# Kernel tuning notes

Hardware: AMD Instinct MI355X
Metric: run time of the kernel (lower is better)

The kernel has to match this reference:

```python
import jax, jax.numpy as jnp
import numpy as np

D_MODEL = 256
NHEAD = 8
HEAD_DIM = D_MODEL // NHEAD
EPS_ATTN = 1e-6
EPS_LN = 1e-5


def _layernorm(x, g, b):
    mu = jnp.mean(x, axis=-1, keepdims=True)
    var = jnp.mean(jnp.square(x - mu), axis=-1, keepdims=True)
    return (x - mu) * jax.lax.rsqrt(var + EPS_LN) * g + b


def _embed_rotary(t, cos, sin):
    # t, cos, sin: [N, L, C]; interleaved pair rotation as in RoFPE.embed_rotary
    t2 = jnp.stack([-t[..., 1::2], t[..., ::2]], axis=-1).reshape(t.shape)
    return t * cos + t2 * sin


def setup_inputs() -> dict:
    key = jax.random.key(0)
    ks = jax.random.split(key, 12)
    N, L, S, C = 4, 4800, 4800, D_MODEL
    w = lambda k, shp: jax.random.normal(k, shp, dtype=jnp.float32) * 0.05
    return {
        "x": jax.random.normal(ks[0], (N, L, C), dtype=jnp.float32),
        "source": jax.random.normal(ks[1], (N, S, C), dtype=jnp.float32),
        "x_pe": jax.random.normal(ks[2], (N, L, C, 2), dtype=jnp.float32),
        "source_pe": jax.random.normal(ks[3], (N, S, C, 2), dtype=jnp.float32),
        "Wq": w(ks[4], (C, C)),
        "Wk": w(ks[5], (C, C)),
        "Wv": w(ks[6], (C, C)),
        "Wm": w(ks[7], (C, C)),
        "W1": w(ks[8], (2 * C, 2 * C)),
        "W2": w(ks[9], (C, 2 * C)),
        "g1": jnp.ones((C,), dtype=jnp.float32),
        "b1": jnp.zeros((C,), dtype=jnp.float32),
        "g2": jnp.ones((C,), dtype=jnp.float32),
        "b2": jnp.zeros((C,), dtype=jnp.float32),
    }


def reference(x, source, x_pe, source_pe, Wq, Wk, Wv, Wm, W1, W2, g1, b1, g2, b2):
    bs, L, C = x.shape
    H, D = NHEAD, HEAD_DIM
    # projections (nn.Linear: y = x @ W.T)
    q = x @ Wq.T
    k = source @ Wk.T
    v = source @ Wv.T
    # inline rotary PE
    q = _embed_rotary(q, x_pe[..., 0], x_pe[..., 1]).reshape(bs, L, H, D)
    k = _embed_rotary(k, source_pe[..., 0], source_pe[..., 1]).reshape(bs, -1, H, D)
    v = v.reshape(bs, -1, H, D)
    # LoFTR linear attention: phi(x) = elu(x) + 1
    Q = jax.nn.elu(q) + 1.0
    K = jax.nn.elu(k) + 1.0
    v_len = v.shape[1]
    vals = v / v_len
    KV = jnp.einsum("nshd,nshv->nhdv", K, vals)          # [N,H,D,D]
    Z = 1.0 / (jnp.einsum("nlhd,nhd->nlh", Q, K.sum(axis=1)) + EPS_ATTN)
    msg = jnp.einsum("nlhd,nhdv,nlh->nlhv", Q, KV, Z) * v_len  # [N,L,H,D]
    # merge + norm1
    msg = msg.reshape(bs, L, H * D) @ Wm.T
    msg = _layernorm(msg, g1, b1)
    # concat-MLP + norm2 + residual
    h = jnp.concatenate([x, msg], axis=-1)               # [N,L,2C]
    h = jax.nn.relu(h @ W1.T) @ W2.T
    h = _layernorm(h, g2, b2)
    return x + h
```

## Files before the change

### kernel.cpp

```cpp
#include <hip/hip_runtime.h>
#include <hip/hip_bf16.h>
#include <math.h>

#define NROWS 19200
#define SLEN  4800
#define KV_CHUNKS 50
#define KV_SC     96

typedef unsigned short ushort_t;
typedef __attribute__((ext_vector_type(8))) short bf16x8;
typedef __attribute__((ext_vector_type(4))) float f32x4;
typedef __attribute__((ext_vector_type(8))) unsigned short ushort8;

__device__ __forceinline__ float bf2f(ushort_t u) {
  union { unsigned int i; float f; } x; x.i = ((unsigned int)u) << 16; return x.f;
}
__device__ __forceinline__ ushort_t f2bf(float f) {
  __hip_bfloat16 h = __float2bfloat16(f);
  union { __hip_bfloat16 h; ushort_t u; } x; x.h = h; return x.u;
}

#define GLOAD16(g, l) __builtin_amdgcn_global_load_lds( \
    (const __attribute__((address_space(1))) unsigned int*)(g), \
    (__attribute__((address_space(3))) unsigned int*)(l), 16, 0, 0)

template <int EPI, bool CONCAT>
__device__ __forceinline__ void gemmT_body(
    const ushort_t* __restrict__ A0, const ushort_t* __restrict__ A1,
    const ushort_t* __restrict__ W, ushort_t* __restrict__ outp,
    int Nn, int K, int bm, int bn, char* smem) {
  const int tid = threadIdx.x;
  const int wave = tid >> 6, lane = tid & 63;
  const int wm = (wave >> 1) * 64, wn = (wave & 1) * 64;
  const int l15 = lane & 15, l4 = lane >> 4;

  f32x4 acc[4][4];
#pragma unroll
  for (int i = 0; i < 4; ++i)
#pragma unroll
    for (int j = 0; j < 4; ++j) acc[i][j] = (f32x4){0.f, 0.f, 0.f, 0.f};

  for (int k0 = 0; k0 < K; k0 += 64) {
    const ushort_t* Asrc;
    int ka;
    if (CONCAT) { Asrc = (k0 < 256) ? A0 : A1; ka = k0 & 255; }
    else        { Asrc = A0; ka = k0; }
#pragma unroll
    for (int c = 0; c < 4; ++c) {
      int ch = c * 4 + wave;
      int o = ch * 1024 + lane * 16;
      int row = o >> 7, g = (o >> 4) & 7;
      const ushort_t* sp =
          Asrc + (size_t)(bm + row) * 256 + ka + ((g ^ (row & 7)) << 3);
      GLOAD16(sp, smem + ch * 1024);
    }
#pragma unroll
    for (int c = 0; c < 4; ++c) {
      int ch = c * 4 + wave;
      int o = ch * 1024 + lane * 16;
      int row = o >> 7, g = (o >> 4) & 7;
      const ushort_t* sp =
          W + (size_t)(bn + row) * K + k0 + ((g ^ (row & 7)) << 3);
      GLOAD16(sp, smem + 16384 + ch * 1024);
    }
    __syncthreads();
#pragma unroll
    for (int kc = 0; kc < 2; ++kc) {
      bf16x8 af[4], bfr[4];
#pragma unroll
      for (int mi = 0; mi < 4; ++mi) {
        int r = wm + mi * 16 + l15;
        int G = kc * 4 + l4;
        af[mi] = *(const bf16x8*)(smem + r * 128 + ((G ^ (r & 7)) << 4));
      }
#pragma unroll
      for (int ni = 0; ni < 4; ++ni) {
        int r = wn + ni * 16 + l15;
        int G = kc * 4 + l4;
        bfr[ni] = *(const bf16x8*)(smem + 16384 + r * 128 +
                                   ((G ^ (r & 7)) << 4));
      }
#pragma unroll
      for (int mi = 0; mi < 4; ++mi)
#pragma unroll
        for (int ni = 0; ni < 4; ++ni)
          acc[mi][ni] = __builtin_amdgcn_mfma_f32_16x16x32_bf16(
              af[mi], bfr[ni], acc[mi][ni], 0, 0, 0);
    }
    __syncthreads();
  }

  ushort_t* st = (ushort_t*)smem;
#pragma unroll
  for (int mi = 0; mi < 4; ++mi)
#pragma unroll
    for (int ni = 0; ni < 4; ++ni)
#pragma unroll
      for (int j = 0; j < 4; ++j) {
        int trow = wm + mi * 16 + l4 * 4 + j;
        int tcol = wn + ni * 16 + l15;
        float v = acc[mi][ni][j];
        if (EPI == 3) v = fmaxf(v, 0.f);
        st[trow * 140 + tcol] = f2bf(v);
      }
  __syncthreads();
#pragma unroll
  for (int c = 0; c < 8; ++c) {
    int ch = c * 256 + tid;
    int row = ch >> 4, g = ch & 15;
    ushort8 u = *(const ushort8*)&st[row * 140 + g * 8];
    *(ushort8*)&outp[(size_t)(bm + row) * Nn + bn + g * 8] = u;
  }
}

__global__ __launch_bounds__(256) void qkv_fused(
    const ushort_t* __restrict__ xb, const ushort_t* __restrict__ srcb,
    const ushort_t* __restrict__ Wqb, const ushort_t* __restrict__ Wkb,
    const ushort_t* __restrict__ Wvb,
    ushort_t* __restrict__ Q, ushort_t* __restrict__ Kb,
    ushort_t* __restrict__ Vb) {
  extern __shared__ char smem[];
  int b = blockIdx.x;
  const int which = b < 300 ? 0 : (b < 600 ? 1 : 2);
  b -= which * 300;
  const int bm = (b >> 1) * 128, bn = (b & 1) * 128;
  const ushort_t* A = (which == 0) ? xb : srcb;
  const ushort_t* W = (which == 0) ? Wqb : (which == 1 ? Wkb : Wvb);
  ushort_t* o = (which == 0) ? Q : (which == 1 ? Kb : Vb);
  gemmT_body<0, false>(A, nullptr, W, o, 256, 256, bm, bn, smem);
}

__global__ __launch_bounds__(256) void mlp1_kernel(
    const ushort_t* __restrict__ xb, const ushort_t* __restrict__ msgln,
    const ushort_t* __restrict__ W1b, ushort_t* __restrict__ h1) {
  extern __shared__ char smem[];
  const int bm = (blockIdx.x >> 2) * 128, bn = (blockIdx.x & 3) * 128;
  gemmT_body<3, true>(xb, msgln, W1b, h1, 512, 512, bm, bn, smem);
}

__global__ __launch_bounds__(256) void msg_merge_ln(
    const ushort_t* __restrict__ Qb, const float* __restrict__ x_pe,
    const float* __restrict__ KV, const float* __restrict__ Ksum,
    const ushort_t* __restrict__ Wm,
    const float* __restrict__ g, const float* __restrict__ bb,
    ushort_t* __restrict__ msgln) {
  __shared__ ushort_t AsM[32 * 256];
  __shared__ ushort_t KVb[8 * 1024];
  __shared__ ushort_t Bs[256 * 32];
  __shared__ float Ks[8][32];
  __shared__ float zS[32][8];
  __shared__ float partS[4][32];
  __shared__ float partQ[4][32];
  __shared__ float gS[256], bS[256];

  const int tid = threadIdx.x;
  const int wave = tid >> 6, lane = tid & 63;
  const int l15 = lane & 15, l4 = lane >> 4;
  const int bm = blockIdx.x * 32;
  const int n = bm / SLEN;

  gS[tid] = g[tid];
  bS[tid] = bb[tid];
  Ks[tid >> 5][tid & 31] = Ksum[(n * 8 + (tid >> 5)) * 32 + (tid & 31)];

#pragma unroll
  for (int c = 0; c < 8; ++c) {
    int e4 = c * 256 + tid;
    const float4 kv4 = *(const float4*)&KV[(size_t)(n * 8) * 1024 + e4 * 4];
    ushort4 u = make_ushort4(f2bf(kv4.x), f2bf(kv4.y), f2bf(kv4.z),
                             f2bf(kv4.w));
    *(ushort4*)&KVb[e4 * 4] = u;
  }

#pragma unroll
  for (int p = 0; p < 4; ++p) {
    int rr = p * 8 + (tid >> 5), cc = (tid & 31) * 8;
    const size_t eoff = (size_t)(bm + rr) * 256 + cc;
    const ushort8 uq = *(const ushort8*)&Qb[eoff];
    const float4* pp = (const float4*)&x_pe[eoff * 2];
    float4 p0 = pp[0], p1 = pp[1], p2 = pp[2], p3 = pp[3];
    float v[8];
#pragma unroll
    for (int i = 0; i < 8; ++i) v[i] = bf2f((ushort_t)uq[i]);
    float r[8];
    r[0] = v[0] * p0.x - v[1] * p0.y; r[1] = v[1] * p0.z + v[0] * p0.w;
    r[2] = v[2] * p1.x - v[3] * p1.y; r[3] = v[3] * p1.z + v[2] * p1.w;
    r[4] = v[4] * p2.x - v[5] * p2.y; r[5] = v[5] * p2.z + v[4] * p2.w;
    r[6] = v[6] * p3.x - v[7] * p3.y; r[7] = v[7] * p3.z + v[6] * p3.w;
    ushort8 pk;
#pragma unroll
    for (int i = 0; i < 8; ++i) {
      float w = r[i] > 0.f ? r[i] + 1.f : __expf(r[i]);
      pk[i] = f2bf(w);
    }
    int gi = cc >> 3;
    int gis = (gi & ~7) | ((gi & 7) ^ (rr & 7));
    *(ushort8*)&AsM[rr * 256 + gis * 8] = pk;
  }
  __syncthreads();

  {
    int row = tid >> 3, h = tid & 7;
    float z = 0.f;
#pragma unroll
    for (int d = 0; d < 32; ++d) {
      int gi = h * 4 + (d >> 3);
      int gis = (gi & ~7) | ((gi & 7) ^ (row & 7));
      z += bf2f(AsM[row * 256 + gis * 8 + (d & 7)]) * Ks[h][d];
    }
    zS[row][h] = 1.0f / (z + 1e-6f);
  }
  __syncthreads();

  f32x4 macc[2][2][2];
#pragma unroll
  for (int hh2 = 0; hh2 < 2; ++hh2) {
    const int h = wave * 2 + hh2;
    bf16x8 af[2], bfr[2];
#pragma unroll
    for (int mi = 0; mi < 2; ++mi) {
      int r = mi * 16 + l15;
      int gi = h * 4 + l4;
      int gis = (gi & ~7) | ((gi & 7) ^ (r & 7));
      af[mi] = *(const bf16x8*)&AsM[r * 256 + gis * 8];
    }
#pragma unroll
    for (int ni = 0; ni < 2; ++ni) {
      int v = ni * 16 + l15;
      const ushort_t* kvb = &KVb[h * 1024 + v];
      bf16x8 t;
#pragma unroll
      for (int i = 0; i < 8; ++i) t[i] = (short)kvb[(l4 * 8 + i) * 32];
      bfr[ni] = t;
    }
#pragma unroll
    for (int mi = 0; mi < 2; ++mi)
#pragma unroll
      for (int ni = 0; ni < 2; ++ni)
        macc[hh2][mi][ni] = __builtin_amdgcn_mfma_f32_16x16x32_bf16(
            af[mi], bfr[ni], (f32x4){0.f, 0.f, 0.f, 0.f}, 0, 0, 0);
  }
  __syncthreads();

#pragma unroll
  for (int hh2 = 0; hh2 < 2; ++hh2) {
    const int h = wave * 2 + hh2;
#pragma unroll
    for (int mi = 0; mi < 2; ++mi)
#pragma unroll
      for (int ni = 0; ni < 2; ++ni)
#pragma unroll
        for (int j = 0; j < 4; ++j) {
          int row = mi * 16 + l4 * 4 + j;
          int col = h * 32 + ni * 16 + l15;
          float mv = macc[hh2][mi][ni][j] * zS[row][h];
          int gi = col >> 3;
          int gis = (gi & ~7) | ((gi & 7) ^ (row & 7));
          AsM[row * 256 + gis * 8 + (col & 7)] = f2bf(mv);
        }
  }
  __syncthreads();

  f32x4 acc[2][4];
#pragma unroll
  for (int i = 0; i < 2; ++i)
#pragma unroll
    for (int j = 0; j < 4; ++j) acc[i][j] = (f32x4){0.f, 0.f, 0.f, 0.f};

  for (int k0 = 0; k0 < 256; k0 += 32) {
#pragma unroll
    for (int c = 0; c < 4; ++c) {
      int ch = c * 256 + tid;
      int row = ch >> 2, gch = ch & 3;
      const ushort_t* src =
          Wm + (size_t)row * 256 + k0 + ((gch ^ (row & 3)) << 3);
      GLOAD16(src, (char*)Bs + ch * 16);
    }
    __syncthreads();
    bf16x8 af[2], bfr[4];
#pragma unroll
    for (int mi = 0; mi < 2; ++mi) {
      int r = mi * 16 + l15;
      int gi = (k0 >> 3) + l4;
      int gis = (gi & ~7) | ((gi & 7) ^ (r & 7));
      af[mi] = *(const bf16x8*)&AsM[r * 256 + gis * 8];
    }
#pragma unroll
    for (int ni = 0; ni < 4; ++ni) {
      int r = wave * 64 + ni * 16 + l15;
      int gs = l4 ^ (r & 3);
      bfr[ni] = *(const bf16x8*)&Bs[r * 32 + gs * 8];
    }
#pragma unroll
    for (int mi = 0; mi < 2; ++mi)
#pragma unroll
      for (int ni = 0; ni < 4; ++ni)
        acc[mi][ni] = __builtin_amdgcn_mfma_f32_16x16x32_bf16(
            af[mi], bfr[ni], acc[mi][ni], 0, 0, 0);
    __syncthreads();
  }

#pragma unroll
  for (int mi = 0; mi < 2; ++mi)
#pragma unroll
    for (int j = 0; j < 4; ++j) {
      float s = acc[mi][0][j] + acc[mi][1][j] + acc[mi][2][j] + acc[mi][3][j];
      float q = acc[mi][0][j] * acc[mi][0][j] + acc[mi][1][j] * acc[mi][1][j] +
                acc[mi][2][j] * acc[mi][2][j] + acc[mi][3][j] * acc[mi][3][j];
#pragma unroll
      for (int m = 1; m < 16; m <<= 1) {
        s += __shfl_xor(s, m);
        q += __shfl_xor(q, m);
      }
      if (l15 == 0) {
        int row = mi * 16 + l4 * 4 + j;
        partS[wave][row] = s;
        partQ[wave][row] = q;
      }
    }
  __syncthreads();

  float mu[2][4], rsv[2][4];
#pragma unroll
  for (int mi = 0; mi < 2; ++mi)
#pragma unroll
    for (int j = 0; j < 4; ++j) {
      int row = mi * 16 + l4 * 4 + j;
      float s = partS[0][row] + partS[1][row] + partS[2][row] + partS[3][row];
      float q2 = partQ[0][row] + partQ[1][row] + partQ[2][row] + partQ[3][row];
      float m_ = s * (1.f / 256.f);
      float var = q2 * (1.f / 256.f) - m_ * m_;
      mu[mi][j] = m_;
      rsv[mi][j] = rsqrtf(var + 1e-5f);
    }

#pragma unroll
  for (int mi = 0; mi < 2; ++mi)
#pragma unroll
    for (int ni = 0; ni < 4; ++ni)
#pragma unroll
      for (int j = 0; j < 4; ++j) {
        int row = mi * 16 + l4 * 4 + j;
        int col2 = wave * 64 + ni * 16 + l15;
        float vv = (acc[mi][ni][j] - mu[mi][j]) * rsv[mi][j] * gS[col2] +
                   bS[col2];
        msgln[(size_t)(bm + row) * 256 + col2] = f2bf(vv);
      }
}

template <int KDIM, bool RESID, bool OUTBF>
__global__ __launch_bounds__(256) void gemm_ln_kernel(
    const ushort_t* __restrict__ A, const ushort_t* __restrict__ W,
    const float* __restrict__ g, const float* __restrict__ bb,
    const float* __restrict__ resid, void* __restrict__ outp) {
  __shared__ char As[32 * 128];
  __shared__ char Bs[256 * 128];
  __shared__ float partS[4][32];
  __shared__ float partQ[4][32];
  __shared__ float gS[256], bS[256];

  const int tid = threadIdx.x;
  const int wave = tid >> 6, lane = tid & 63;
  const int l15 = lane & 15, l4 = lane >> 4;
  const int bm = blockIdx.x * 32;

  gS[tid] = g[tid];
  bS[tid] = bb[tid];

  f32x4 acc[2][4];
#pragma unroll
  for (int i = 0; i < 2; ++i)
#pragma unroll
    for (int j = 0; j < 4; ++j) acc[i][j] = (f32x4){0.f, 0.f, 0.f, 0.f};

  for (int k0 = 0; k0 < KDIM; k0 += 64) {
    {
      int row = tid >> 3, gch = tid & 7;
      const ushort_t* src =
          A + (size_t)(bm + row) * KDIM + k0 + ((gch ^ (row & 7)) << 3);
      GLOAD16(src, As + tid * 16);
    }
#pragma unroll
    for (int c = 0; c < 8; ++c) {
      int ch = c * 256 + tid;
      int row = ch >> 3, gch = ch & 7;
      const ushort_t* src =
          W + (size_t)row * KDIM + k0 + ((gch ^ (row & 7)) << 3);
      GLOAD16(src, Bs + ch * 16);
    }
    __syncthreads();
#pragma unroll
    for (int kc = 0; kc < 2; ++kc) {
      bf16x8 af[2], bfr[4];
#pragma unroll
      for (int mi = 0; mi < 2; ++mi) {
        int r = mi * 16 + l15;
        int G = kc * 4 + l4;
        af[mi] = *(const bf16x8*)(As + r * 128 + ((G ^ (r & 7)) << 4));
      }
#pragma unroll
      for (int ni = 0; ni < 4; ++ni) {
        int r = wave * 64 + ni * 16 + l15;
        int G = kc * 4 + l4;
        bfr[ni] = *(const bf16x8*)(Bs + r * 128 + ((G ^ (r & 7)) << 4));
      }
#pragma unroll
      for (int mi = 0; mi < 2; ++mi)
#pragma unroll
        for (int ni = 0; ni < 4; ++ni)
          acc[mi][ni] = __builtin_amdgcn_mfma_f32_16x16x32_bf16(
              af[mi], bfr[ni], acc[mi][ni], 0, 0, 0);
    }
    __syncthreads();
  }

#pragma unroll
  for (int mi = 0; mi < 2; ++mi)
#pragma unroll
    for (int j = 0; j < 4; ++j) {
      float s = acc[mi][0][j] + acc[mi][1][j] + acc[mi][2][j] + acc[mi][3][j];
      float q = acc[mi][0][j] * acc[mi][0][j] + acc[mi][1][j] * acc[mi][1][j] +
                acc[mi][2][j] * acc[mi][2][j] + acc[mi][3][j] * acc[mi][3][j];
#pragma unroll
      for (int m = 1; m < 16; m <<= 1) {
        s += __shfl_xor(s, m);
        q += __shfl_xor(q, m);
      }
      if (l15 == 0) {
        int row = mi * 16 + l4 * 4 + j;
        partS[wave][row] = s;
        partQ[wave][row] = q;
      }
    }
  __syncthreads();

  float mu[2][4], rsv[2][4];
#pragma unroll
  for (int mi = 0; mi < 2; ++mi)
#pragma unroll
    for (int j = 0; j < 4; ++j) {
      int row = mi * 16 + l4 * 4 + j;
      float s = partS[0][row] + partS[1][row] + partS[2][row] + partS[3][row];
      float q2 = partQ[0][row] + partQ[1][row] + partQ[2][row] + partQ[3][row];
      float m_ = s * (1.f / 256.f);
      float var = q2 * (1.f / 256.f) - m_ * m_;
      mu[mi][j] = m_;
      rsv[mi][j] = rsqrtf(var + 1e-5f);
    }

#pragma unroll
  for (int mi = 0; mi < 2; ++mi)
#pragma unroll
    for (int ni = 0; ni < 4; ++ni)
#pragma unroll
      for (int j = 0; j < 4; ++j) {
        int row = mi * 16 + l4 * 4 + j;
        int col = wave * 64 + ni * 16 + l15;
        float v = (acc[mi][ni][j] - mu[mi][j]) * rsv[mi][j] * gS[col] + bS[col];
        size_t gr = (size_t)(bm + row);
        if (RESID) v += resid[gr * 256 + col];
        if (OUTBF)
          ((ushort_t*)outp)[gr * 256 + col] = f2bf(v);
        else
          ((float*)outp)[gr * 256 + col] = v;
      }
}

__global__ __launch_bounds__(256) void kv_partial(
    const ushort_t* __restrict__ Kb, const ushort_t* __restrict__ Vb,
    const float* __restrict__ s_pe,
    float* __restrict__ kvp, float* __restrict__ ksp) {
  __shared__ float bufK[32][32];
  __shared__ float bufV[32][32];
  const int b = blockIdx.x;
  const int ch = b % KV_CHUNKS;
  const int nh = b / KV_CHUNKS;
  const int h = nh & 7, n = nh >> 3;
  const int tid = threadIdx.x;
  const int d = tid >> 3, vb = (tid & 7) * 4;
  const int half = tid >> 7, t = tid & 127;
  const int srow = t >> 2, seg = (t & 3) * 8;
  const int segS = (seg + 8 * (srow & 3)) & 31;
  float a0 = 0.f, a1 = 0.f, a2 = 0.f, a3 = 0.f, ks = 0.f;
  const size_t base = (size_t)n * SLEN * 256 + (size_t)h * 32;
  const int s0 = ch * KV_SC;
  for (int s = s0; s < s0 + KV_SC; s += 32) {
    __syncthreads();
    const size_t eoff = base + (size_t)(s + srow) * 256 + seg;
    ushort8 u = *(const ushort8*)((half ? Vb : Kb) + eoff);
    float v[8];
#pragma unroll
    for (int i = 0; i < 8; ++i) v[i] = bf2f((ushort_t)u[i]);
    if (!half) {
      const float4* pp = (const float4*)&s_pe[eoff * 2];
      float4 p0 = pp[0], p1 = pp[1], p2 = pp[2], p3 = pp[3];
      float r[8];
      r[0] = v[0] * p0.x - v[1] * p0.y; r[1] = v[1] * p0.z + v[0] * p0.w;
      r[2] = v[2] * p1.x - v[3] * p1.y; r[3] = v[3] * p1.z + v[2] * p1.w;
      r[4] = v[4] * p2.x - v[5] * p2.y; r[5] = v[5] * p2.z + v[4] * p2.w;
      r[6] = v[6] * p3.x - v[7] * p3.y; r[7] = v[7] * p3.z + v[6] * p3.w;
#pragma unroll
      for (int i = 0; i < 8; ++i)
        v[i] = r[i] > 0.f ? r[i] + 1.f : __expf(r[i]);
    }
    float* dst = half ? &bufV[srow][segS] : &bufK[srow][segS];
    *(float4*)dst = (float4){v[0], v[1], v[2], v[3]};
    *(float4*)(dst + 4) = (float4){v[4], v[5], v[6], v[7]};
    __syncthreads();
#pragma unroll
    for (int ss = 0; ss < 32; ++ss) {
      int rot = 8 * (ss & 3);
      float kd = bufK[ss][(d + rot) & 31];
      float4 vv = *(const float4*)&bufV[ss][(vb + rot) & 31];
      a0 += kd * vv.x; a1 += kd * vv.y; a2 += kd * vv.z; a3 += kd * vv.w;
      ks += kd;
    }
  }
  float* kv = &kvp[(size_t)b * 1024 + d * 32 + vb];
  kv[0] = a0; kv[1] = a1; kv[2] = a2; kv[3] = a3;
  if ((tid & 7) == 0) ksp[(size_t)b * 32 + d] = ks;
}

__global__ __launch_bounds__(256) void kv_reduce(
    const float* __restrict__ kvp, const float* __restrict__ ksp,
    float* __restrict__ KV, float* __restrict__ Ksum) {
  const int nh = blockIdx.x;
  const int tid = threadIdx.x;
  for (int e = tid; e < 1024; e += 256) {
    float s = 0.f;
    for (int p = 0; p < KV_CHUNKS; ++p)
      s += kvp[(size_t)(nh * KV_CHUNKS + p) * 1024 + e];
    KV[(size_t)nh * 1024 + e] = s;
  }
  if (tid < 32) {
    float s = 0.f;
    for (int p = 0; p < KV_CHUNKS; ++p)
      s += ksp[(size_t)(nh * KV_CHUNKS + p) * 32 + tid];
    Ksum[nh * 32 + tid] = s;
  }
}

__global__ __launch_bounds__(256) void conv_all(
    const float* __restrict__ x, const float* __restrict__ src,
    const float* w0, const float* w1, const float* w2, const float* w3,
    const float* w4, const float* w5,
    ushort_t* __restrict__ xo, ushort_t* __restrict__ so,
    ushort_t* o0, ushort_t* o1, ushort_t* o2, ushort_t* o3, ushort_t* o4,
    ushort_t* o5) {
  int blk = blockIdx.x;
  if (blk < 4800) {
    const float* s; ushort_t* d;
    if (blk < 2400) { s = x; d = xo; } else { s = src; d = so; blk -= 2400; }
    size_t o = ((size_t)blk * 256 + threadIdx.x) * 8;
    float4 v0 = *(const float4*)&s[o];
    float4 v1 = *(const float4*)&s[o + 4];
    ushort8 u = {f2bf(v0.x), f2bf(v0.y), f2bf(v0.z), f2bf(v0.w),
                 f2bf(v1.x), f2bf(v1.y), f2bf(v1.z), f2bf(v1.w)};
    *(ushort8*)&d[o] = u;
  } else {
    int e = ((blk - 4800) * 256 + threadIdx.x) * 4;
    const float* s; ushort_t* d; int off;
    if      (e < 65536)  { s = w0; d = o0; off = e; }
    else if (e < 131072) { s = w1; d = o1; off = e - 65536; }
    else if (e < 196608) { s = w2; d = o2; off = e - 131072; }
    else if (e < 262144) { s = w3; d = o3; off = e - 196608; }
    else if (e < 524288) { s = w4; d = o4; off = e - 262144; }
    else                 { s = w5; d = o5; off = e - 524288; }
    float4 v = *(const float4*)&s[off];
    ushort4 u = make_ushort4(f2bf(v.x), f2bf(v.y), f2bf(v.z), f2bf(v.w));
    *(ushort4*)&d[off] = u;
  }
}

extern "C" void kernel_launch(void* const* d_in, const int* in_sizes, int n_in,
                              void* d_out, int out_size, void* d_ws,
                              size_t ws_size, hipStream_t stream) {
  const float* x    = (const float*)d_in[0];
  const float* src  = (const float*)d_in[1];
  const float* x_pe = (const float*)d_in[2];
  const float* s_pe = (const float*)d_in[3];
  const float* Wq = (const float*)d_in[4];
  const float* Wk = (const float*)d_in[5];
  const float* Wv = (const float*)d_in[6];
  const float* Wm = (const float*)d_in[7];
  const float* W1 = (const float*)d_in[8];
  const float* W2 = (const float*)d_in[9];
  const float* g1 = (const float*)d_in[10];
  const float* b1 = (const float*)d_in[11];
  const float* g2 = (const float*)d_in[12];
  const float* b2 = (const float*)d_in[13];
  float* out = (float*)d_out;

  const size_t R = (size_t)NROWS * 256;
  ushort_t* xb    = (ushort_t*)d_ws;
  ushort_t* srcb  = xb + R;
  ushort_t* Qb    = srcb + R;
  ushort_t* Kb    = Qb + R;
  ushort_t* Vb    = Kb + R;
  ushort_t* msgln = Vb + R;
  ushort_t* Wqb   = msgln + R;
  ushort_t* Wkb   = Wqb + 65536;
  ushort_t* Wvb   = Wkb + 65536;
  ushort_t* Wmb   = Wvb + 65536;
  ushort_t* W1b   = Wmb + 65536;
  ushort_t* W2b   = W1b + 262144;
  float* kvp      = (float*)(W2b + 131072);
  float* ksp      = kvp + 1638400;
  float* KVb      = ksp + 51200;
  float* Ksum     = KVb + 32768;
  ushort_t* h1   = Kb;

  dim3 blk(256);
  conv_all<<<5440, blk, 0, stream>>>(x, src, Wq, Wk, Wv, Wm, W1, W2,
                                     xb, srcb, Wqb, Wkb, Wvb, Wmb, W1b, W2b);
  qkv_fused<<<900, blk, 35840, stream>>>(xb, srcb, Wqb, Wkb, Wvb, Qb, Kb, Vb);
  kv_partial<<<1600, blk, 0, stream>>>(Kb, Vb, s_pe, kvp, ksp);
  kv_reduce<<<32, blk, 0, stream>>>(kvp, ksp, KVb, Ksum);
  msg_merge_ln<<<600, blk, 0, stream>>>(Qb, x_pe, KVb, Ksum, Wmb, g1, b1,
                                        msgln);
  mlp1_kernel<<<600, blk, 35840, stream>>>(xb, msgln, W1b, h1);
  gemm_ln_kernel<512, true, false><<<600, blk, 0, stream>>>(
      h1, W2b, g2, b2, x, out);
}
```

Measured before the change: 121.8 us.

## Transpose KV in reduce, vectorize KV fragment loads, fuse Z, widen Wm k-tile

kv_reduce now writes KV transposed, so msg_merge_ln can store it swizzled in LDS and load each MFMA B fragment with one 16-byte read instead of eight strided scalar reads. The Z normalizer is computed from the fp32 phi values in registers with a shuffle reduction, which removes an LDS pass and a barrier. The Wm GEMM loop uses 64-wide k tiles, halving its iteration and barrier count, and reuses one shared buffer for both KV and the Wm tiles. The barrier before the first Wm load is removed, so correctness relies on the aliased buffer already being past its KV reads.

```diff
diff --git a/kernel.cpp b/kernel.cpp
--- a/kernel.cpp
+++ b/kernel.cpp
@@ -140,13 +140,12 @@
 
 __global__ __launch_bounds__(256) void msg_merge_ln(
     const ushort_t* __restrict__ Qb, const float* __restrict__ x_pe,
-    const float* __restrict__ KV, const float* __restrict__ Ksum,
+    const float* __restrict__ KVt, const float* __restrict__ Ksum,
     const ushort_t* __restrict__ Wm,
     const float* __restrict__ g, const float* __restrict__ bb,
     ushort_t* __restrict__ msgln) {
   __shared__ ushort_t AsM[32 * 256];
-  __shared__ ushort_t KVb[8 * 1024];
-  __shared__ ushort_t Bs[256 * 32];
+  __shared__ ushort_t U[256 * 64];
   __shared__ float Ks[8][32];
   __shared__ float zS[32][8];
   __shared__ float partS[4][32];
@@ -163,13 +162,17 @@
   bS[tid] = bb[tid];
   Ks[tid >> 5][tid & 31] = Ksum[(n * 8 + (tid >> 5)) * 32 + (tid & 31)];
 
+  ushort_t* KVl = U;
 #pragma unroll
   for (int c = 0; c < 8; ++c) {
     int e4 = c * 256 + tid;
-    const float4 kv4 = *(const float4*)&KV[(size_t)(n * 8) * 1024 + e4 * 4];
+    const float4 kv4 = *(const float4*)&KVt[(size_t)(n * 8) * 1024 + e4 * 4];
+    int E = e4 * 4;
+    int h = E >> 10, v = (E >> 5) & 31, d0 = E & 31;
+    int gsw = (d0 >> 3) ^ ((v >> 1) & 3);
     ushort4 u = make_ushort4(f2bf(kv4.x), f2bf(kv4.y), f2bf(kv4.z),
                              f2bf(kv4.w));
-    *(ushort4*)&KVb[e4 * 4] = u;
+    *(ushort4*)&KVl[h * 1024 + v * 32 + gsw * 8 + (d0 & 7)] = u;
   }
 
 #pragma unroll
@@ -187,28 +190,24 @@
     r[2] = v[2] * p1.x - v[3] * p1.y; r[3] = v[3] * p1.z + v[2] * p1.w;
     r[4] = v[4] * p2.x - v[5] * p2.y; r[5] = v[5] * p2.z + v[4] * p2.w;
     r[6] = v[6] * p3.x - v[7] * p3.y; r[7] = v[7] * p3.z + v[6] * p3.w;
+    float w[8];
     ushort8 pk;
 #pragma unroll
     for (int i = 0; i < 8; ++i) {
-      float w = r[i] > 0.f ? r[i] + 1.f : __expf(r[i]);
-      pk[i] = f2bf(w);
+      w[i] = r[i] > 0.f ? r[i] + 1.f : __expf(r[i]);
+      pk[i] = f2bf(w[i]);
     }
     int gi = cc >> 3;
     int gis = (gi & ~7) | ((gi & 7) ^ (rr & 7));
     *(ushort8*)&AsM[rr * 256 + gis * 8] = pk;
-  }
-  __syncthreads();
-
-  {
-    int row = tid >> 3, h = tid & 7;
-    float z = 0.f;
-#pragma unroll
-    for (int d = 0; d < 32; ++d) {
-      int gi = h * 4 + (d >> 3);
-      int gis = (gi & ~7) | ((gi & 7) ^ (row & 7));
-      z += bf2f(AsM[row * 256 + gis * 8 + (d & 7)]) * Ks[h][d];
-    }
-    zS[row][h] = 1.0f / (z + 1e-6f);
+    const int hh = (tid & 31) >> 2;
+    const int db = (tid & 3) * 8;
+    float zp = 0.f;
+#pragma unroll
+    for (int i = 0; i < 8; ++i) zp += w[i] * Ks[hh][db + i];
+    zp += __shfl_xor(zp, 1);
+    zp += __shfl_xor(zp, 2);
+    if ((tid & 3) == 0) zS[rr][hh] = 1.0f / (zp + 1e-6f);
   }
   __syncthreads();
 
@@ -227,11 +226,8 @@
 #pragma unroll
     for (int ni = 0; ni < 2; ++ni) {
       int v = ni * 16 + l15;
-      const ushort_t* kvb = &KVb[h * 1024 + v];
-      bf16x8 t;
-#pragma unroll
-      for (int i = 0; i < 8; ++i) t[i] = (short)kvb[(l4 * 8 + i) * 32];
-      bfr[ni] = t;
+      int gsw = l4 ^ ((v >> 1) & 3);
+      bfr[ni] = *(const bf16x8*)&KVl[h * 1024 + v * 32 + gsw * 8];
     }
 #pragma unroll
     for (int mi = 0; mi < 2; ++mi)
@@ -259,44 +255,47 @@
           AsM[row * 256 + gis * 8 + (col & 7)] = f2bf(mv);
         }
   }
-  __syncthreads();
-
+
+  ushort_t* Bs = U;
   f32x4 acc[2][4];
 #pragma unroll
   for (int i = 0; i < 2; ++i)
 #pragma unroll
     for (int j = 0; j < 4; ++j) acc[i][j] = (f32x4){0.f, 0.f, 0.f, 0.f};
 
-  for (int k0 = 0; k0 < 256; k0 += 32) {
-#pragma unroll
-    for (int c = 0; c < 4; ++c) {
+  for (int k0 = 0; k0 < 256; k0 += 64) {
+#pragma unroll
+    for (int c = 0; c < 8; ++c) {
       int ch = c * 256 + tid;
-      int row = ch >> 2, gch = ch & 3;
+      int row = ch >> 3, gch = ch & 7;
       const ushort_t* src =
-          Wm + (size_t)row * 256 + k0 + ((gch ^ (row & 3)) << 3);
+          Wm + (size_t)row * 256 + k0 + ((gch ^ (row & 7)) << 3);
       GLOAD16(src, (char*)Bs + ch * 16);
     }
     __syncthreads();
-    bf16x8 af[2], bfr[4];
-#pragma unroll
-    for (int mi = 0; mi < 2; ++mi) {
-      int r = mi * 16 + l15;
-      int gi = (k0 >> 3) + l4;
-      int gis = (gi & ~7) | ((gi & 7) ^ (r & 7));
-      af[mi] = *(const bf16x8*)&AsM[r * 256 + gis * 8];
-    }
-#pragma unroll
-    for (int ni = 0; ni < 4; ++ni) {
-      int r = wave * 64 + ni * 16 + l15;
-      int gs = l4 ^ (r & 3);
-      bfr[ni] = *(const bf16x8*)&Bs[r * 32 + gs * 8];
-    }
-#pragma unroll
-    for (int mi = 0; mi < 2; ++mi)
-#pragma unroll
-      for (int ni = 0; ni < 4; ++ni)
-        acc[mi][ni] = __builtin_amdgcn_mfma_f32_16x16x32_bf16(
-            af[mi], bfr[ni], acc[mi][ni], 0, 0, 0);
+#pragma unroll
+    for (int kc = 0; kc < 2; ++kc) {
+      bf16x8 af[2], bfr[4];
+#pragma unroll
+      for (int mi = 0; mi < 2; ++mi) {
+        int r = mi * 16 + l15;
+        int gi = (k0 >> 3) + kc * 4 + l4;
+        int gis = (gi & ~7) | ((gi & 7) ^ (r & 7));
+        af[mi] = *(const bf16x8*)&AsM[r * 256 + gis * 8];
+      }
+#pragma unroll
+      for (int ni = 0; ni < 4; ++ni) {
+        int r = wave * 64 + ni * 16 + l15;
+        int G = kc * 4 + l4;
+        bfr[ni] = *(const bf16x8*)((char*)Bs + r * 128 + ((G ^ (r & 7)) << 4));
+      }
+#pragma unroll
+      for (int mi = 0; mi < 2; ++mi)
+#pragma unroll
+        for (int ni = 0; ni < 4; ++ni)
+          acc[mi][ni] = __builtin_amdgcn_mfma_f32_16x16x32_bf16(
+              af[mi], bfr[ni], acc[mi][ni], 0, 0, 0);
+    }
     __syncthreads();
   }
 
@@ -523,14 +522,14 @@
 
 __global__ __launch_bounds__(256) void kv_reduce(
     const float* __restrict__ kvp, const float* __restrict__ ksp,
-    float* __restrict__ KV, float* __restrict__ Ksum) {
+    float* __restrict__ KVt, float* __restrict__ Ksum) {
   const int nh = blockIdx.x;
   const int tid = threadIdx.x;
   for (int e = tid; e < 1024; e += 256) {
     float s = 0.f;
     for (int p = 0; p < KV_CHUNKS; ++p)
       s += kvp[(size_t)(nh * KV_CHUNKS + p) * 1024 + e];
-    KV[(size_t)nh * 1024 + e] = s;
+    KVt[(size_t)nh * 1024 + (e & 31) * 32 + (e >> 5)] = s;
   }
   if (tid < 32) {
     float s = 0.f;
@@ -606,8 +605,8 @@
   ushort_t* W2b   = W1b + 262144;
   float* kvp      = (float*)(W2b + 131072);
   float* ksp      = kvp + 1638400;
-  float* KVb      = ksp + 51200;
-  float* Ksum     = KVb + 32768;
+  float* KVt      = ksp + 51200;
+  float* Ksum     = KVt + 32768;
   ushort_t* h1   = Kb;
 
   dim3 blk(256);
@@ -615,8 +614,8 @@
                                      xb, srcb, Wqb, Wkb, Wvb, Wmb, W1b, W2b);
   qkv_fused<<<900, blk, 35840, stream>>>(xb, srcb, Wqb, Wkb, Wvb, Qb, Kb, Vb);
   kv_partial<<<1600, blk, 0, stream>>>(Kb, Vb, s_pe, kvp, ksp);
-  kv_reduce<<<32, blk, 0, stream>>>(kvp, ksp, KVb, Ksum);
-  msg_merge_ln<<<600, blk, 0, stream>>>(Qb, x_pe, KVb, Ksum, Wmb, g1, b1,
+  kv_reduce<<<32, blk, 0, stream>>>(kvp, ksp, KVt, Ksum);
+  msg_merge_ln<<<600, blk, 0, stream>>>(Qb, x_pe, KVt, Ksum, Wmb, g1, b1,
                                         msgln);
   mlp1_kernel<<<600, blk, 35840, stream>>>(xb, msgln, W1b, h1);
   gemm_ln_kernel<512, true, false><<<600, blk, 0, stream>>>(
```

Result: no change. 119.6 us (-1.8%).
